# Kernel tuning notes

Hardware: AMD Instinct MI355X
Metric: run time of the kernel (lower is better)

Reference implementation:

```python
import jax, jax.numpy as jnp
import numpy as np
from jax import lax

DIM = 256
HEADS = 8
C3 = DIM * 3 // 4  # 192
C1 = DIM // 4      # 64


def conv1x1(x, w):
    # x: [b,c,h,w], w: [o,c] (1x1 conv, no bias)
    return jnp.einsum('bchw,oc->bohw', x, w)


def dwconv3x3(x, w):
    # x: [b,c,h,w], w: [c,1,3,3] depthwise
    return lax.conv_general_dilated(
        x, w, window_strides=(1, 1), padding='SAME',
        feature_group_count=x.shape[1],
        dimension_numbers=('NCHW', 'OIHW', 'NCHW'))


def l2norm(x, eps=1e-12):
    # torch F.normalize: x / max(||x||, eps) along last dim
    n = jnp.sqrt(jnp.sum(x * x, axis=-1, keepdims=True))
    return x / jnp.maximum(n, eps)


def setup_inputs() -> dict:
    key = jax.random.key(0)
    ks = jax.random.split(key, 10)
    s = 0.02
    return {
        'x': jax.random.normal(ks[0], (4, DIM, 128, 128), jnp.float32),
        'k_v': jax.random.normal(ks[1], (4, 256), jnp.float32),
        'temperature': jnp.ones((HEADS, 1, 1), jnp.float32),
        'w_kR': jax.random.normal(ks[2], (C3, 192), jnp.float32) * s,
        'w_kI': jax.random.normal(ks[3], (C1, 64), jnp.float32) * s,
        'w_qR': jax.random.normal(ks[4], (DIM, C3), jnp.float32) * s,
        'w_qdw': jax.random.normal(ks[5], (DIM, 1, 3, 3), jnp.float32) * s,
        'w_kvI': jax.random.normal(ks[6], (2 * DIM, C1), jnp.float32) * s,
        'w_kvdw': jax.random.normal(ks[7], (2 * DIM, 1, 3, 3), jnp.float32) * s,
        'w_proj': jax.random.normal(ks[8], (DIM, DIM), jnp.float32) * s,
    }


def reference(x, k_v, temperature, w_kR, w_kI, w_qR, w_qdw, w_kvI, w_kvdw, w_proj):
    b, c, h, w = x.shape
    # FiLM-style modulation: x * kv + x
    kvr = (k_v[:, :192] @ w_kR.T)[:, :, None, None]  # [b, C3, 1, 1]
    kvi = (k_v[:, 192:] @ w_kI.T)[:, :, None, None]  # [b, C1, 1, 1]
    x_r = x[:, :C3] * kvr + x[:, :C3]
    x_i = x[:, C3:] * kvi + x[:, C3:]
    # QKV projections
    q = dwconv3x3(conv1x1(x_r, w_qR), w_qdw)          # [b, dim, h, w]
    kv = dwconv3x3(conv1x1(x_i, w_kvI), w_kvdw)       # [b, 2*dim, h, w]
    k, v = jnp.split(kv, 2, axis=1)
    hd = DIM // HEADS
    hw = h * w
    q = q.reshape(b, HEADS, hd, hw)
    k = k.reshape(b, HEADS, hd, hw)
    v = v.reshape(b, HEADS, hd, hw)
    # channel-wise (transposed) attention with L2 norm + temperature
    q = l2norm(q)
    k = l2norm(k)
    attn = jnp.einsum('bhcn,bhdn->bhcd', q, k) * temperature  # [b,H,hd,hd]
    attn = jax.nn.softmax(attn, axis=-1)
    out = jnp.einsum('bhcd,bhdn->bhcn', attn, v)
    out = out.reshape(b, DIM, h, w)
    return conv1x1(out, w_proj)
```

## Files before the change

### kernel.cpp

```cpp
#include <hip/hip_runtime.h>
#include <math.h>

#define HW 16384

typedef unsigned int uint;
typedef short bfrag __attribute__((ext_vector_type(8)));
typedef float f32x4 __attribute__((ext_vector_type(4)));

union FragCvt { uint4 u; bfrag v; };

__device__ inline uint pack2bf(float a, float b) {
  uint ua = __builtin_bit_cast(uint, a);
  uint ub = __builtin_bit_cast(uint, b);
  ua = (ua + 0x7FFFu + ((ua >> 16) & 1u)) >> 16;
  ub = (ub + 0x7FFFu + ((ub >> 16) & 1u)) & 0xFFFF0000u;
  return ua | ub;
}

__global__ __launch_bounds__(256) void mod_kernel(
    const float* __restrict__ kv, const float* __restrict__ wkR,
    const float* __restrict__ wkI, float* __restrict__ mod)
{
  int b = blockIdx.x;
  int c = threadIdx.x;
  const float* kvb = kv + b * 256;
  float s = 0.f;
  if (c < 192) {
    const float* wr = wkR + c * 192;
    for (int j = 0; j < 192; ++j) s += kvb[j] * wr[j];
  } else {
    const float* wi = wkI + (c - 192) * 64;
    for (int j = 0; j < 64; ++j) s += kvb[192 + j] * wi[j];
  }
  mod[b * 256 + c] = 1.f + s;
}

__global__ __launch_bounds__(256) void mgemm(
    const float* __restrict__ W, int ldW, size_t Wbstride,
    const float* __restrict__ X, int c0, size_t Xbstride,
    const float* __restrict__ mod,
    float* __restrict__ Y, size_t Ybstride, int K)
{
  int b = blockIdx.z, mt = blockIdx.y, nt = blockIdx.x;
  const float* Wb = W + (size_t)b * Wbstride + (size_t)mt * 128 * ldW;
  const float* Xb = X + (size_t)b * Xbstride + (size_t)c0 * HW + nt * 128;
  float* Yb = Y + (size_t)b * Ybstride + (size_t)mt * 128 * HW + nt * 128;

  __shared__ unsigned short Al[128 * 40];
  __shared__ unsigned short Bl[128 * 40];

  int t = threadIdx.x;
  int w = t >> 6, l = t & 63;
  int wm = (w >> 1) * 64, wn = (w & 1) * 64;
  int lm = l & 15, lk = (l >> 4) * 8;

  int am = t >> 1, ako = (t & 1) * 16;
  int bn = t & 127, bo = (t >> 7) * 8;

  f32x4 acc[4][4];
  #pragma unroll
  for (int fi = 0; fi < 4; ++fi)
    #pragma unroll
    for (int fj = 0; fj < 4; ++fj) acc[fi][fj] = {0.f, 0.f, 0.f, 0.f};

  for (int k0 = 0; k0 < K; k0 += 32) {
    const float* wsrc = Wb + (size_t)am * ldW + k0 + ako;
    float4 a0 = *(const float4*)(wsrc);
    float4 a1 = *(const float4*)(wsrc + 4);
    float4 a2 = *(const float4*)(wsrc + 8);
    float4 a3 = *(const float4*)(wsrc + 12);

    float xr[2][8];
    #pragma unroll
    for (int i = 0; i < 2; ++i) {
      int kb = k0 + bo + i * 16;
      #pragma unroll
      for (int r = 0; r < 8; ++r)
        xr[i][r] = Xb[(size_t)(kb + r) * HW + bn];
    }
    float sc[2][8];
    if (mod) {
      const float* mp = mod + b * 256 + c0 + k0 + bo;
      #pragma unroll
      for (int i = 0; i < 2; ++i) {
        float4 m0 = *(const float4*)(mp + i * 16);
        float4 m1 = *(const float4*)(mp + i * 16 + 4);
        sc[i][0] = m0.x; sc[i][1] = m0.y; sc[i][2] = m0.z; sc[i][3] = m0.w;
        sc[i][4] = m1.x; sc[i][5] = m1.y; sc[i][6] = m1.z; sc[i][7] = m1.w;
      }
    } else {
      #pragma unroll
      for (int i = 0; i < 2; ++i)
        #pragma unroll
        for (int r = 0; r < 8; ++r) sc[i][r] = 1.f;
    }

    __syncthreads();

    uint4 aw0, aw1;
    aw0.x = pack2bf(a0.x, a0.y); aw0.y = pack2bf(a0.z, a0.w);
    aw0.z = pack2bf(a1.x, a1.y); aw0.w = pack2bf(a1.z, a1.w);
    aw1.x = pack2bf(a2.x, a2.y); aw1.y = pack2bf(a2.z, a2.w);
    aw1.z = pack2bf(a3.x, a3.y); aw1.w = pack2bf(a3.z, a3.w);
    *(uint4*)&Al[am * 40 + ako] = aw0;
    *(uint4*)&Al[am * 40 + ako + 8] = aw1;

    #pragma unroll
    for (int i = 0; i < 2; ++i) {
      uint4 bw;
      bw.x = pack2bf(xr[i][0] * sc[i][0], xr[i][1] * sc[i][1]);
      bw.y = pack2bf(xr[i][2] * sc[i][2], xr[i][3] * sc[i][3]);
      bw.z = pack2bf(xr[i][4] * sc[i][4], xr[i][5] * sc[i][5]);
      bw.w = pack2bf(xr[i][6] * sc[i][6], xr[i][7] * sc[i][7]);
      *(uint4*)&Bl[bn * 40 + bo + i * 16] = bw;
    }

    __syncthreads();

    bfrag af[4], bfr[4];
    #pragma unroll
    for (int fi = 0; fi < 4; ++fi) {
      FragCvt cv;
      cv.u = *(const uint4*)&Al[(wm + fi * 16 + lm) * 40 + lk];
      af[fi] = cv.v;
    }
    #pragma unroll
    for (int fj = 0; fj < 4; ++fj) {
      FragCvt cv;
      cv.u = *(const uint4*)&Bl[(wn + fj * 16 + lm) * 40 + lk];
      bfr[fj] = cv.v;
    }
    #pragma unroll
    for (int fi = 0; fi < 4; ++fi)
      #pragma unroll
      for (int fj = 0; fj < 4; ++fj)
        acc[fi][fj] = __builtin_amdgcn_mfma_f32_16x16x32_bf16(
            af[fi], bfr[fj], acc[fi][fj], 0, 0, 0);
  }

  int orow = (l >> 4) * 4;
  #pragma unroll
  for (int fi = 0; fi < 4; ++fi)
    #pragma unroll
    for (int fj = 0; fj < 4; ++fj)
      #pragma unroll
      for (int r = 0; r < 4; ++r)
        Yb[(size_t)(wm + fi * 16 + orow + r) * HW + (wn + fj * 16 + lm)] =
            acc[fi][fj][r];
}

__global__ __launch_bounds__(256) void dwconv_kernel(
    const float* __restrict__ in, size_t in_bstride,
    const float* __restrict__ wdw,
    float* __restrict__ out, size_t out_bstride,
    float* __restrict__ ssq)
{
  int c = blockIdx.x;
  int b = blockIdx.y;
  int t = threadIdx.x;
  int r = t >> 5;
  int xq = t & 31;

  const float4* ip4 = (const float4*)(in + (size_t)b * in_bstride + ((size_t)c << 14));
  float4* op4 = (float4*)(out + (size_t)b * out_bstride + ((size_t)c << 14));
  const float* wp = wdw + c * 9;
  float w0 = wp[0], w1 = wp[1], w2 = wp[2], w3 = wp[3], w4 = wp[4],
        w5 = wp[5], w6 = wp[6], w7 = wp[7], w8 = wp[8];

  const float4 z4 = make_float4(0.f, 0.f, 0.f, 0.f);
  int y0 = r << 4;

  float4 a = (y0 > 0) ? ip4[((y0 - 1) << 5) + xq] : z4;
  float4 bb = ip4[(y0 << 5) + xq];

  float aL = __shfl_up(a.w, 1);  if (xq == 0)  aL = 0.f;
  float aR = __shfl_down(a.x, 1); if (xq == 31) aR = 0.f;
  float bL = __shfl_up(bb.w, 1); if (xq == 0)  bL = 0.f;
  float bR = __shfl_down(bb.x, 1); if (xq == 31) bR = 0.f;

  float ss = 0.f;
  #pragma unroll
  for (int i = 0; i < 16; ++i) {
    int y = y0 + i;
    int yc = (y + 1 < 128) ? (y + 1) : 127;
    float4 cc = ip4[(yc << 5) + xq];
    if (y + 1 >= 128) { cc.x = 0.f; cc.y = 0.f; cc.z = 0.f; cc.w = 0.f; }
    float cL = __shfl_up(cc.w, 1);  if (xq == 0)  cL = 0.f;
    float cR = __shfl_down(cc.x, 1); if (xq == 31) cR = 0.f;

    float4 o;
    o.x = w0 * aL  + w1 * a.x + w2 * a.y +
          w3 * bL  + w4 * bb.x + w5 * bb.y +
          w6 * cL  + w7 * cc.x + w8 * cc.y;
    o.y = w0 * a.x + w1 * a.y + w2 * a.z +
          w3 * bb.x + w4 * bb.y + w5 * bb.z +
          w6 * cc.x + w7 * cc.y + w8 * cc.z;
    o.z = w0 * a.y + w1 * a.z + w2 * a.w +
          w3 * bb.y + w4 * bb.z + w5 * bb.w +
          w6 * cc.y + w7 * cc.z + w8 * cc.w;
    o.w = w0 * a.z + w1 * a.w + w2 * aR +
          w3 * bb.z + w4 * bb.w + w5 * bR +
          w6 * cc.z + w7 * cc.w + w8 * cR;

    op4[(y << 5) + xq] = o;
    ss += o.x * o.x + o.y * o.y + o.z * o.z + o.w * o.w;

    a = bb; aL = bL; aR = bR;
    bb = cc; bL = cL; bR = cR;
  }

  if (ssq) {
    #pragma unroll
    for (int off = 32; off > 0; off >>= 1) ss += __shfl_down(ss, off);
    __shared__ float red[4];
    if ((t & 63) == 0) red[t >> 6] = ss;
    __syncthreads();
    if (t == 0) ssq[b * 256 + c] = red[0] + red[1] + red[2] + red[3];
  }
}

__global__ __launch_bounds__(256) void gram_kernel(
    const float* __restrict__ qdw, const float* __restrict__ kdw,
    float* __restrict__ S)
{
  int chunk = blockIdx.x, h = blockIdx.y, b = blockIdx.z;
  __shared__ float Qs[32][68];
  __shared__ float Ks[32][68];
  int t = threadIdx.x;
  int wave = t >> 6, lane = t & 63;
  int c0 = lane >> 3, d0 = lane & 7;
  float acc[4][4];
  #pragma unroll
  for (int i = 0; i < 4; ++i)
    #pragma unroll
    for (int j = 0; j < 4; ++j) acc[i][j] = 0.f;

  const float* qb = qdw + (((size_t)b * 256 + h * 32) << 14) + chunk * 1024;
  const float* kb = kdw + (((size_t)b * 256 + h * 32) << 14) + chunk * 1024;
  int lch = t >> 4;
  int lpx = (t & 15) << 2;

  for (int sub = 0; sub < 16; ++sub) {
    float4 qa = *(const float4*)(qb + ((size_t)lch << 14) + sub * 64 + lpx);
    float4 qc = *(const float4*)(qb + ((size_t)(lch + 16) << 14) + sub * 64 + lpx);
    float4 ka = *(const float4*)(kb + ((size_t)lch << 14) + sub * 64 + lpx);
    float4 kc = *(const float4*)(kb + ((size_t)(lch + 16) << 14) + sub * 64 + lpx);
    __syncthreads();
    *(float4*)&Qs[lch][lpx] = qa;
    *(float4*)&Qs[lch + 16][lpx] = qc;
    *(float4*)&Ks[lch][lpx] = ka;
    *(float4*)&Ks[lch + 16][lpx] = kc;
    __syncthreads();
    #pragma unroll
    for (int pg = 0; pg < 4; ++pg) {
      int p0 = (wave << 4) + (pg << 2);
      float4 q0 = *(float4*)&Qs[c0][p0];
      float4 q1 = *(float4*)&Qs[c0 + 8][p0];
      float4 q2 = *(float4*)&Qs[c0 + 16][p0];
      float4 q3 = *(float4*)&Qs[c0 + 24][p0];
      float4 k0v = *(float4*)&Ks[d0][p0];
      float4 k1v = *(float4*)&Ks[d0 + 8][p0];
      float4 k2v = *(float4*)&Ks[d0 + 16][p0];
      float4 k3v = *(float4*)&Ks[d0 + 24][p0];
      float qv[4][4] = {{q0.x, q0.y, q0.z, q0.w}, {q1.x, q1.y, q1.z, q1.w},
                        {q2.x, q2.y, q2.z, q2.w}, {q3.x, q3.y, q3.z, q3.w}};
      float kv[4][4] = {{k0v.x, k0v.y, k0v.z, k0v.w}, {k1v.x, k1v.y, k1v.z, k1v.w},
                        {k2v.x, k2v.y, k2v.z, k2v.w}, {k3v.x, k3v.y, k3v.z, k3v.w}};
      #pragma unroll
      for (int i = 0; i < 4; ++i)
        #pragma unroll
        for (int j = 0; j < 4; ++j)
          acc[i][j] += qv[i][0] * kv[j][0] + qv[i][1] * kv[j][1] +
                       qv[i][2] * kv[j][2] + qv[i][3] * kv[j][3];
    }
  }
  float* Sp = S + (((size_t)b * 8 + h) << 10);
  #pragma unroll
  for (int i = 0; i < 4; ++i)
    #pragma unroll
    for (int j = 0; j < 4; ++j)
      atomicAdd(&Sp[(c0 + 8 * i) * 32 + d0 + 8 * j], acc[i][j]);
}

__global__ __launch_bounds__(64) void softmax_kernel(
    float* __restrict__ S, const float* __restrict__ ssq,
    const float* __restrict__ ssk, const float* __restrict__ temp)
{
  int bh = blockIdx.x;
  int b = bh >> 3, h = bh & 7;
  int c = threadIdx.x;
  if (c >= 32) return;
  float* row = S + ((size_t)bh << 10) + c * 32;
  float invq = 1.f / fmaxf(sqrtf(ssq[b * 256 + h * 32 + c]), 1e-12f);
  float T = temp[h];
  float lg[32];
  float mx = -1e30f;
  for (int d = 0; d < 32; ++d) {
    float invk = 1.f / fmaxf(sqrtf(ssk[b * 256 + h * 32 + d]), 1e-12f);
    float v = row[d] * invq * invk * T;
    lg[d] = v;
    mx = fmaxf(mx, v);
  }
  float sum = 0.f;
  for (int d = 0; d < 32; ++d) { float e = expf(lg[d] - mx); lg[d] = e; sum += e; }
  float inv = 1.f / sum;
  for (int d = 0; d < 32; ++d) row[d] = lg[d] * inv;
}

__global__ __launch_bounds__(256) void mbuild_kernel(
    const float* __restrict__ attn, const float* __restrict__ wproj,
    float* __restrict__ M)
{
  int o = blockIdx.x, b = blockIdx.y;
  int col = threadIdx.x;
  int h = col >> 5, d = col & 31;
  const float* a = attn + (((size_t)b * 8 + h) << 10);
  const float* wp = wproj + o * 256 + h * 32;
  float s = 0.f;
  #pragma unroll
  for (int cc = 0; cc < 32; ++cc) s += wp[cc] * a[cc * 32 + d];
  M[((size_t)b * 256 + o) * 256 + col] = s;
}

extern "C" void kernel_launch(void* const* d_in, const int* in_sizes, int n_in,
                              void* d_out, int out_size, void* d_ws, size_t ws_size,
                              hipStream_t stream)
{
  const float* x      = (const float*)d_in[0];
  const float* k_v    = (const float*)d_in[1];
  const float* temp   = (const float*)d_in[2];
  const float* w_kR   = (const float*)d_in[3];
  const float* w_kI   = (const float*)d_in[4];
  const float* w_qR   = (const float*)d_in[5];
  const float* w_qdw  = (const float*)d_in[6];
  const float* w_kvI  = (const float*)d_in[7];
  const float* w_kvdw = (const float*)d_in[8];
  const float* w_proj = (const float*)d_in[9];
  float* out = (float*)d_out;

  float* ws   = (float*)d_ws;
  float* bufA = ws;
  float* bufB = ws + 16777216;
  float* bufC = ws + 33554432;
  float* sm   = ws + 50331648;
  float* mod  = sm;
  float* ssq  = sm + 1024;
  float* ssk  = sm + 2048;
  float* S    = sm + 3072;
  float* M    = sm + 3072 + 32768;

  hipMemsetAsync(S, 0, (size_t)32768 * sizeof(float), stream);

  mod_kernel<<<dim3(4), dim3(256), 0, stream>>>(k_v, w_kR, w_kI, mod);

  mgemm<<<dim3(128, 2, 4), dim3(256), 0, stream>>>(
      w_kvI, 64, 0, x, 192, 4194304, mod, bufA, 4194304, 64);
  dwconv_kernel<<<dim3(256, 4), dim3(256), 0, stream>>>(
      bufA, 4194304, w_kvdw, bufB, 4194304, ssk);

  mgemm<<<dim3(128, 2, 4), dim3(256), 0, stream>>>(
      w_qR, 192, 0, x, 0, 4194304, mod, bufA, 4194304, 192);
  dwconv_kernel<<<dim3(256, 4), dim3(256), 0, stream>>>(
      bufA, 4194304, w_qdw, bufC, 4194304, ssq);

  gram_kernel<<<dim3(16, 8, 4), dim3(256), 0, stream>>>(bufC, bufB, S);

  mgemm<<<dim3(128, 2, 4), dim3(256), 0, stream>>>(
      w_kvI + 256 * 64, 64, 0, x, 192, 4194304, mod, bufA, 4194304, 64);

  softmax_kernel<<<dim3(32), dim3(64), 0, stream>>>(S, ssq, ssk, temp);
  mbuild_kernel<<<dim3(256, 4), dim3(256), 0, stream>>>(S, w_proj, M);

  dwconv_kernel<<<dim3(256, 4), dim3(256), 0, stream>>>(
      bufA, 4194304, w_kvdw + 256 * 9, bufC, 4194304, (float*)nullptr);

  mgemm<<<dim3(128, 2, 4), dim3(256), 0, stream>>>(
      M, 256, 65536, bufC, 0, 4194304, (const float*)nullptr, out, 4194304, 256);
}
```

Baseline: 335.2 us.

## Compute Q·K Gram matrix with split-bf16 MFMA instead of scalar FMA

Rewrites the gram kernel to load Q and K directly from global memory into registers. Each fp32 value is split into bf16 high and low parts, and the partial Gram matrix is accumulated with 16x16x32 bf16 MFMA instructions using three products (hi*hi, hi*lo, lo*hi) to keep close to fp32 accuracy. Per-wave results are reduced in shared memory before one atomicAdd per element, where before each thread issued 16 atomics. This removes the shared-memory staging and scalar FMA work, at the cost of conversion ALU work and slightly reduced precision.

Result: no change. 333.7 us (-0.4%).

```diff
diff --git a/kernel.cpp b/kernel.cpp
--- a/kernel.cpp
+++ b/kernel.cpp
@@ -15,6 +15,25 @@
   ua = (ua + 0x7FFFu + ((ua >> 16) & 1u)) >> 16;
   ub = (ub + 0x7FFFu + ((ub >> 16) & 1u)) & 0xFFFF0000u;
   return ua | ub;
+}
+
+__device__ inline void cvt_hilo(float4 a, float4 b, bfrag& hi, bfrag& lo) {
+  float v0[8] = {a.x, a.y, a.z, a.w, b.x, b.y, b.z, b.w};
+  uint hv[4], lv[4];
+  #pragma unroll
+  for (int i = 0; i < 4; ++i) {
+    float x0 = v0[2 * i], x1 = v0[2 * i + 1];
+    uint h = pack2bf(x0, x1);
+    float h0 = __builtin_bit_cast(float, h << 16);
+    float h1 = __builtin_bit_cast(float, h & 0xFFFF0000u);
+    hv[i] = h;
+    lv[i] = pack2bf(x0 - h0, x1 - h1);
+  }
+  FragCvt ch, cl;
+  ch.u = make_uint4(hv[0], hv[1], hv[2], hv[3]);
+  cl.u = make_uint4(lv[0], lv[1], lv[2], lv[3]);
+  hi = ch.v;
+  lo = cl.v;
 }
 
 __global__ __launch_bounds__(256) void mod_kernel(
@@ -224,62 +243,74 @@
     float* __restrict__ S)
 {
   int chunk = blockIdx.x, h = blockIdx.y, b = blockIdx.z;
-  __shared__ float Qs[32][68];
-  __shared__ float Ks[32][68];
   int t = threadIdx.x;
-  int wave = t >> 6, lane = t & 63;
-  int c0 = lane >> 3, d0 = lane & 7;
-  float acc[4][4];
-  #pragma unroll
-  for (int i = 0; i < 4; ++i)
-    #pragma unroll
-    for (int j = 0; j < 4; ++j) acc[i][j] = 0.f;
-
-  const float* qb = qdw + (((size_t)b * 256 + h * 32) << 14) + chunk * 1024;
-  const float* kb = kdw + (((size_t)b * 256 + h * 32) << 14) + chunk * 1024;
-  int lch = t >> 4;
-  int lpx = (t & 15) << 2;
-
-  for (int sub = 0; sub < 16; ++sub) {
-    float4 qa = *(const float4*)(qb + ((size_t)lch << 14) + sub * 64 + lpx);
-    float4 qc = *(const float4*)(qb + ((size_t)(lch + 16) << 14) + sub * 64 + lpx);
-    float4 ka = *(const float4*)(kb + ((size_t)lch << 14) + sub * 64 + lpx);
-    float4 kc = *(const float4*)(kb + ((size_t)(lch + 16) << 14) + sub * 64 + lpx);
-    __syncthreads();
-    *(float4*)&Qs[lch][lpx] = qa;
-    *(float4*)&Qs[lch + 16][lpx] = qc;
-    *(float4*)&Ks[lch][lpx] = ka;
-    *(float4*)&Ks[lch + 16][lpx] = kc;
-    __syncthreads();
-    #pragma unroll
-    for (int pg = 0; pg < 4; ++pg) {
-      int p0 = (wave << 4) + (pg << 2);
-      float4 q0 = *(float4*)&Qs[c0][p0];
-      float4 q1 = *(float4*)&Qs[c0 + 8][p0];
-      float4 q2 = *(float4*)&Qs[c0 + 16][p0];
-      float4 q3 = *(float4*)&Qs[c0 + 24][p0];
-      float4 k0v = *(float4*)&Ks[d0][p0];
-      float4 k1v = *(float4*)&Ks[d0 + 8][p0];
-      float4 k2v = *(float4*)&Ks[d0 + 16][p0];
-      float4 k3v = *(float4*)&Ks[d0 + 24][p0];
-      float qv[4][4] = {{q0.x, q0.y, q0.z, q0.w}, {q1.x, q1.y, q1.z, q1.w},
-                        {q2.x, q2.y, q2.z, q2.w}, {q3.x, q3.y, q3.z, q3.w}};
-      float kv[4][4] = {{k0v.x, k0v.y, k0v.z, k0v.w}, {k1v.x, k1v.y, k1v.z, k1v.w},
-                        {k2v.x, k2v.y, k2v.z, k2v.w}, {k3v.x, k3v.y, k3v.z, k3v.w}};
-      #pragma unroll
-      for (int i = 0; i < 4; ++i)
-        #pragma unroll
-        for (int j = 0; j < 4; ++j)
-          acc[i][j] += qv[i][0] * kv[j][0] + qv[i][1] * kv[j][1] +
-                       qv[i][2] * kv[j][2] + qv[i][3] * kv[j][3];
-    }
-  }
+  int w = t >> 6, l = t & 63;
+  int lm = l & 15;
+  int lk8 = (l >> 4) * 8;
+
+  const float* qh = qdw + (((size_t)b * 256 + h * 32) << 14);
+  const float* kh = kdw + (((size_t)b * 256 + h * 32) << 14);
+  const float* q0 = qh + ((size_t)lm << 14);
+  const float* q1 = q0 + ((size_t)16 << 14);
+  const float* k0 = kh + ((size_t)lm << 14);
+  const float* k1 = k0 + ((size_t)16 << 14);
+
+  int px0 = chunk * 1024 + w * 256 + lk8;
+
+  f32x4 acc[2][2], accl[2][2];
+  #pragma unroll
+  for (int mi = 0; mi < 2; ++mi)
+    #pragma unroll
+    for (int nj = 0; nj < 2; ++nj) {
+      acc[mi][nj] = {0.f, 0.f, 0.f, 0.f};
+      accl[mi][nj] = {0.f, 0.f, 0.f, 0.f};
+    }
+
+  #pragma unroll 2
+  for (int s = 0; s < 8; ++s) {
+    int px = px0 + s * 32;
+    float4 a0 = *(const float4*)(q0 + px);
+    float4 a1 = *(const float4*)(q0 + px + 4);
+    float4 a2 = *(const float4*)(q1 + px);
+    float4 a3 = *(const float4*)(q1 + px + 4);
+    float4 b0 = *(const float4*)(k0 + px);
+    float4 b1 = *(const float4*)(k0 + px + 4);
+    float4 b2 = *(const float4*)(k1 + px);
+    float4 b3 = *(const float4*)(k1 + px + 4);
+
+    bfrag qhF[2], qlF[2], khF[2], klF[2];
+    cvt_hilo(a0, a1, qhF[0], qlF[0]);
+    cvt_hilo(a2, a3, qhF[1], qlF[1]);
+    cvt_hilo(b0, b1, khF[0], klF[0]);
+    cvt_hilo(b2, b3, khF[1], klF[1]);
+
+    #pragma unroll
+    for (int mi = 0; mi < 2; ++mi)
+      #pragma unroll
+      for (int nj = 0; nj < 2; ++nj) {
+        acc[mi][nj] = __builtin_amdgcn_mfma_f32_16x16x32_bf16(
+            qhF[mi], khF[nj], acc[mi][nj], 0, 0, 0);
+        accl[mi][nj] = __builtin_amdgcn_mfma_f32_16x16x32_bf16(
+            qhF[mi], klF[nj], accl[mi][nj], 0, 0, 0);
+        accl[mi][nj] = __builtin_amdgcn_mfma_f32_16x16x32_bf16(
+            qlF[mi], khF[nj], accl[mi][nj], 0, 0, 0);
+      }
+  }
+
+  __shared__ float red[4][1024];
+  int orow = (l >> 4) * 4;
+  #pragma unroll
+  for (int mi = 0; mi < 2; ++mi)
+    #pragma unroll
+    for (int nj = 0; nj < 2; ++nj)
+      #pragma unroll
+      for (int r = 0; r < 4; ++r)
+        red[w][(mi * 16 + orow + r) * 32 + nj * 16 + lm] =
+            acc[mi][nj][r] + accl[mi][nj][r];
+  __syncthreads();
   float* Sp = S + (((size_t)b * 8 + h) << 10);
-  #pragma unroll
-  for (int i = 0; i < 4; ++i)
-    #pragma unroll
-    for (int j = 0; j < 4; ++j)
-      atomicAdd(&Sp[(c0 + 8 * i) * 32 + d0 + 8 * j], acc[i][j]);
+  for (int idx = t; idx < 1024; idx += 256)
+    atomicAdd(&Sp[idx], red[0][idx] + red[1][idx] + red[2][idx] + red[3][idx]);
 }
 
 __global__ __launch_bounds__(64) void softmax_kernel(
```
